# Kernel tuning notes

Hardware: AMD Instinct MI355X
Metric: run time of the kernel (lower is better)

The kernel has to match this reference:

```python
import jax, jax.numpy as jnp
import numpy as np

B, S, D_MODEL = 2, 2048, 2048
N_HEADS, N_KV_HEADS = 32, 8
HEAD_DIM = D_MODEL // N_HEADS  # 64


def setup_inputs() -> dict:
    key = jax.random.key(0)
    ks = jax.random.split(key, 7)
    # rope frequencies (as in standard RoPE; values just need to be the right shape)
    inv_freq = 1.0 / (10000.0 ** (jnp.arange(0, HEAD_DIM, 2, dtype=jnp.float32) / HEAD_DIM))
    t = jnp.arange(S, dtype=jnp.float32)
    freqs = t[:, None] * inv_freq[None, :]  # (S, head_dim//2)
    scale = 0.02
    return {
        "x": jax.random.normal(ks[0], (B, S, D_MODEL), jnp.float32),
        "cos": jnp.cos(freqs),
        "sin": jnp.sin(freqs),
        "Wq": jax.random.normal(ks[1], (N_HEADS * HEAD_DIM, D_MODEL), jnp.float32) * scale,
        "Wk": jax.random.normal(ks[2], (N_KV_HEADS * HEAD_DIM, D_MODEL), jnp.float32) * scale,
        "Wv": jax.random.normal(ks[3], (N_KV_HEADS * HEAD_DIM, D_MODEL), jnp.float32) * scale,
        "Wo": jax.random.normal(ks[4], (D_MODEL, D_MODEL), jnp.float32) * scale,
    }


def _apply_rope(x, cos, sin):
    # x: (B, H, S, D); cos/sin: (S, D//2)
    d = x.shape[-1]
    x1, x2 = x[..., : d // 2], x[..., d // 2:]
    c = cos[None, None]
    s = sin[None, None]
    return jnp.concatenate([x1 * c - x2 * s, x1 * s + x2 * c], axis=-1)


def reference(x, cos, sin, Wq, Wk, Wv, Wo):
    b, s, _ = x.shape
    hd = 2 * cos.shape[-1]
    h = Wq.shape[0] // hd
    kv = Wk.shape[0] // hd
    g = h // kv  # query heads per kv head

    q = (x @ Wq.T).reshape(b, s, h, hd).transpose(0, 2, 1, 3)    # (b,h,s,d)
    k = (x @ Wk.T).reshape(b, s, kv, hd).transpose(0, 2, 1, 3)   # (b,kv,s,d)
    v = (x @ Wv.T).reshape(b, s, kv, hd).transpose(0, 2, 1, 3)

    q = _apply_rope(q, cos, sin)
    k = _apply_rope(k, cos, sin)

    # GQA: group query heads instead of materializing repeated K/V
    qg = q.reshape(b, kv, g, s, hd)
    scale = 1.0 / jnp.sqrt(jnp.asarray(hd, x.dtype))
    scores = jnp.einsum('bkgsd,bktd->bkgst', qg, k) * scale      # (b,kv,g,s,s)
    causal = jnp.arange(s)[:, None] >= jnp.arange(s)[None, :]
    scores = jnp.where(causal[None, None, None], scores, jnp.asarray(-jnp.inf, scores.dtype))
    attn = jax.nn.softmax(scores, axis=-1)
    out = jnp.einsum('bkgst,bktd->bkgsd', attn, v)               # (b,kv,g,s,d)
    out = out.reshape(b, h, s, hd).transpose(0, 2, 1, 3).reshape(b, s, h * hd)
    return out @ Wo.T
```

## Files before the change

### kernel.cpp

```cpp
#include <hip/hip_runtime.h>
#include <hip/hip_bf16.h>

typedef __bf16 bf16;
typedef __attribute__((ext_vector_type(8))) __bf16 bf16x8;
typedef __attribute__((ext_vector_type(4))) __bf16 bf16x4;
typedef __attribute__((ext_vector_type(4))) float f32x4;

#define B_SZ 2
#define S_SZ 2048
#define D_SZ 2048
#define H_SZ 32
#define KV_SZ 8
#define HD_SZ 64
#define M_SZ (B_SZ * S_SZ)
#define NQKV 3072

#define GLDS(g, s) __builtin_amdgcn_global_load_lds( \
    (const __attribute__((address_space(1))) void*)(g), \
    (__attribute__((address_space(3))) void*)(s), 16, 0, 0)

__global__ void cvt_all(const float* __restrict__ x, const float* __restrict__ Wq,
                        const float* __restrict__ Wk, const float* __restrict__ Wv,
                        const float* __restrict__ Wo,
                        bf16* __restrict__ xb, bf16* __restrict__ Wf, bf16* __restrict__ wob,
                        int nx, int n1, int n2) {
    int i = blockIdx.x * blockDim.x + threadIdx.x;
    const float* src; bf16* dst; int off;
    if (i < nx)                 { src = x;  dst = xb; off = i; }
    else {
        int j = i - nx;
        if (j < n1)             { src = Wq; dst = Wf; off = j; }
        else if (j < n1 + n2)   { src = Wk; dst = Wf + (size_t)4 * n1; off = j - n1; }
        else if (j < n1 + 2*n2) { src = Wv; dst = Wf + (size_t)4 * (n1 + n2); off = j - n1 - n2; }
        else if (j < 2*n1+2*n2) { src = Wo; dst = wob; off = j - n1 - 2 * n2; }
        else return;
    }
    float4 v = ((const float4*)src)[off];
    bf16x4 o;
    o.x = (bf16)v.x; o.y = (bf16)v.y; o.z = (bf16)v.z; o.w = (bf16)v.w;
    ((bf16x4*)dst)[off] = o;
}

#define GEMM_CORE2(A_, B_, Kdim)                                                 \
    const int tid  = threadIdx.x;                                                \
    const int w    = tid >> 6;                                                   \
    const int lane = tid & 63;                                                   \
    const int c = lane & 15, quad = lane >> 4;                                   \
    const int g8 = lane >> 3;                                                    \
    const int chs = ((lane & 7) ^ g8) * 8;                                       \
    const int rowBase = blockIdx.y * 128;                                        \
    const int colBase = blockIdx.x * 128;                                        \
    const bf16* Ag = A_ + (size_t)(rowBase + w * 64 + g8) * Kdim + chs;          \
    const bf16* Bg = B_ + (size_t)(colBase + w * 64 + g8) * Kdim + chs;          \
    bf16* sAw = As + (w * 64) * 64;                                              \
    bf16* sBw = Bs + (w * 64) * 64;                                              \
    f32x4 acc[4][8] = {};                                                        \
    for (int k0 = 0; k0 < Kdim; k0 += 64) {                                      \
        _Pragma("unroll")                                                        \
        for (int j = 0; j < 8; j++) {                                            \
            GLDS(Ag + (size_t)(j * 8) * Kdim + k0, sAw + j * 512);               \
            GLDS(Bg + (size_t)(j * 8) * Kdim + k0, sBw + j * 512);               \
        }                                                                        \
        __syncthreads();                                                         \
        _Pragma("unroll")                                                        \
        for (int ks = 0; ks < 2; ks++) {                                         \
            bf16x8 af[4], bfr[8];                                                \
            _Pragma("unroll")                                                    \
            for (int mi = 0; mi < 4; mi++)                                       \
                af[mi] = *(const bf16x8*)(As + (w * 64 + mi * 16 + c) * 64       \
                                          + (((ks << 2) + quad) ^ (c & 7)) * 8); \
            _Pragma("unroll")                                                    \
            for (int ni = 0; ni < 8; ni++)                                       \
                bfr[ni] = *(const bf16x8*)(Bs + (ni * 16 + c) * 64               \
                                          + (((ks << 2) + quad) ^ (c & 7)) * 8); \
            _Pragma("unroll")                                                    \
            for (int mi = 0; mi < 4; mi++)                                       \
                _Pragma("unroll")                                                \
                for (int ni = 0; ni < 8; ni++)                                   \
                    acc[mi][ni] = __builtin_amdgcn_mfma_f32_16x16x32_bf16(       \
                        af[mi], bfr[ni], acc[mi][ni], 0, 0, 0);                  \
        }                                                                        \
        __syncthreads();                                                         \
    }                                                                            \
    const int mBase = rowBase + w * 64;

__global__ __launch_bounds__(128, 2)
void gemm_qkv(const bf16* __restrict__ A, const bf16* __restrict__ Bw,
              bf16* __restrict__ Qb, bf16* __restrict__ Kb, bf16* __restrict__ Vtb,
              const float* __restrict__ cosp, const float* __restrict__ sinp,
              float qscale)
{
    __shared__ __align__(16) bf16 As[128 * 64];
    __shared__ __align__(16) bf16 Bs[128 * 64];

    GEMM_CORE2(A, Bw, D_SZ)

#pragma unroll
    for (int half = 0; half < 2; half++) {
        const int hcol = colBase + half * 64;
        const int no   = half * 4;
        if (hcol < 2560) {
            bf16* dst; int hh, Hn; float sc;
            if (hcol < 2048) { dst = Qb; hh = hcol >> 6;        Hn = H_SZ;  sc = qscale; }
            else             { dst = Kb; hh = (hcol >> 6) - 32; Hn = KV_SZ; sc = 1.0f;  }
#pragma unroll
            for (int mi = 0; mi < 4; mi++) {
#pragma unroll
                for (int r = 0; r < 4; r++) {
                    int row = mBase + mi * 16 + quad * 4 + r;
                    int b = row >> 11;
                    int s = row & 2047;
                    const float* cr = cosp + (size_t)s * 32;
                    const float* sr = sinp + (size_t)s * 32;
                    size_t base = ((size_t)(b * Hn + hh) * S_SZ + s) * 64;
#pragma unroll
                    for (int nj = 0; nj < 2; nj++) {
                        int d = nj * 16 + c;
                        float x1 = acc[mi][no + nj][r];
                        float x2 = acc[mi][no + nj + 2][r];
                        float cv = cr[d], sv = sr[d];
                        dst[base + d]      = (bf16)((x1 * cv - x2 * sv) * sc);
                        dst[base + d + 32] = (bf16)((x1 * sv + x2 * cv) * sc);
                    }
                }
            }
        } else {
            const int kvh = (hcol >> 6) - 40;
            const int b   = mBase >> 11;
            const int s0  = mBase & 2047;
#pragma unroll
            for (int nj = 0; nj < 4; nj++) {
                int d = nj * 16 + c;
                size_t base = ((size_t)(b * KV_SZ + kvh) * 64 + d) * (size_t)S_SZ;
#pragma unroll
                for (int mi = 0; mi < 4; mi++) {
                    int s = s0 + mi * 16 + quad * 4;
#pragma unroll
                    for (int r = 0; r < 4; r++)
                        Vtb[base + s + r] = (bf16)acc[mi][no + nj][r];
                }
            }
        }
    }
}

__global__ __launch_bounds__(128, 2)
void gemm_out(const bf16* __restrict__ A, const bf16* __restrict__ Bw,
              float* __restrict__ Co, int N, int K)
{
    __shared__ __align__(16) bf16 As[128 * 64];
    __shared__ __align__(16) bf16 Bs[128 * 64];

    GEMM_CORE2(A, Bw, K)

#pragma unroll
    for (int mi = 0; mi < 4; mi++)
#pragma unroll
        for (int ni = 0; ni < 8; ni++) {
            int col = colBase + ni * 16 + c;
#pragma unroll
            for (int r = 0; r < 4; r++) {
                int row = mBase + mi * 16 + quad * 4 + r;
                Co[(size_t)row * N + col] = acc[mi][ni][r];
            }
        }
}

#define PST 72

__global__ __launch_bounds__(256, 3)
void flash_attn(const bf16* __restrict__ Q, const bf16* __restrict__ Kc,
                const bf16* __restrict__ Vt, bf16* __restrict__ Aout)
{
    __shared__ __align__(16) bf16 Ks[64 * 64];
    __shared__ __align__(16) bf16 Vs[64 * 64];
    __shared__ __align__(16) bf16 Ps[2 * 4 * 16 * PST];

    const int tid  = threadIdx.x;
    const int lane = tid & 63;
    const int wave = tid >> 6;
    const int c = lane & 15, quad = lane >> 4;
    const int qloc = wave * 16 + c;

    const int i  = blockIdx.x;
    const int tA = 31 - i, tB = i;
    const int q0A = tA << 6, q0B = tB << 6;

    const int bh = blockIdx.y;
    const int b  = bh >> 5;
    const int h  = bh & 31;
    const int kv = h >> 2;

    const bf16* Qp = Q  + (size_t)bh * (S_SZ * 64);
    const bf16* Kp = Kc + (size_t)(b * KV_SZ + kv) * (S_SZ * 64);
    const bf16* Vp = Vt + (size_t)(b * KV_SZ + kv) * (64 * S_SZ);

    bf16x8 aqA[2], aqB[2];
    {
        const bf16* qa = Qp + (size_t)(q0A + qloc) * 64 + quad * 8;
        aqA[0] = *(const bf16x8*)qa;  aqA[1] = *(const bf16x8*)(qa + 32);
        const bf16* qb = Qp + (size_t)(q0B + qloc) * 64 + quad * 8;
        aqB[0] = *(const bf16x8*)qb;  aqB[1] = *(const bf16x8*)(qb + 32);
    }

    f32x4 oA[4] = {}, oB[4] = {};
    f32x4 lA = {}, lB = {};

    bf16x8 ones;
#pragma unroll
    for (int j = 0; j < 8; j++) ones[j] = (bf16)1.0f;

    const int srow = tid >> 3;
    const int ch   = tid & 7;
    const int sws  = (ch ^ (srow & 7)) * 8;
    const bf16* Kg0 = Kp + (size_t)srow * 64 + ch * 8;
    const bf16* Kg1 = Kp + (size_t)(srow + 32) * 64 + ch * 8;
    const bf16* Vg0 = Vp + (size_t)srow * S_SZ + ch * 8;
    const bf16* Vg1 = Vp + (size_t)(srow + 32) * S_SZ + ch * 8;

    uint4 pk0 = *(const uint4*)Kg0, pk1 = *(const uint4*)Kg1;
    uint4 pv0 = *(const uint4*)Vg0, pv1 = *(const uint4*)Vg1;

    bf16* PwA = Ps + wave * 16 * PST;
    bf16* PwB = Ps + (4 + wave) * 16 * PST;

    for (int kt = 0; kt <= tA; kt++) {
        *(uint4*)(Ks + srow * 64 + sws)        = pk0;
        *(uint4*)(Ks + (srow + 32) * 64 + sws) = pk1;
        *(uint4*)(Vs + srow * 64 + sws)        = pv0;
        *(uint4*)(Vs + (srow + 32) * 64 + sws) = pv1;
        __syncthreads();
        if (kt < tA) {
            pk0 = *(const uint4*)(Kg0 + (size_t)(kt + 1) * 4096);
            pk1 = *(const uint4*)(Kg1 + (size_t)(kt + 1) * 4096);
            pv0 = *(const uint4*)(Vg0 + (kt + 1) * 64);
            pv1 = *(const uint4*)(Vg1 + (kt + 1) * 64);
        }

        bf16x8 ak[2][4], av[2][4];
#pragma unroll
        for (int ks = 0; ks < 2; ks++)
#pragma unroll
            for (int ni = 0; ni < 4; ni++) {
                const int co = (((ks << 2) + quad) ^ (c & 7)) * 8;
                ak[ks][ni] = *(const bf16x8*)(Ks + (ni * 16 + c) * 64 + co);
                av[ks][ni] = *(const bf16x8*)(Vs + (ni * 16 + c) * 64 + co);
            }

        const bool diagA = (kt == tA);
        const bool doB   = (kt <= tB);
        const bool diagB = (kt == tB);

        {
            f32x4 sc[4] = {};
#pragma unroll
            for (int ks = 0; ks < 2; ks++)
#pragma unroll
                for (int ni = 0; ni < 4; ni++)
                    sc[ni] = __builtin_amdgcn_mfma_f32_16x16x32_bf16(ak[ks][ni], aqA[ks], sc[ni], 0, 0, 0);
#pragma unroll
            for (int ni = 0; ni < 4; ni++) {
                bf16x4 pk;
#pragma unroll
                for (int r = 0; r < 4; r++) {
                    float p = exp2f(sc[ni][r]);
                    if (diagA && (ni * 16 + quad * 4 + r) > qloc) p = 0.f;
                    pk[r] = (bf16)p;
                }
                *(bf16x4*)(PwA + c * PST + ni * 16 + quad * 4) = pk;
            }
#pragma unroll
            for (int ks = 0; ks < 2; ks++) {
                bf16x8 bp = *(const bf16x8*)(PwA + c * PST + ks * 32 + quad * 8);
                lA = __builtin_amdgcn_mfma_f32_16x16x32_bf16(ones, bp, lA, 0, 0, 0);
#pragma unroll
                for (int ni = 0; ni < 4; ni++)
                    oA[ni] = __builtin_amdgcn_mfma_f32_16x16x32_bf16(av[ks][ni], bp, oA[ni], 0, 0, 0);
            }
        }
        if (doB) {
            f32x4 sc[4] = {};
#pragma unroll
            for (int ks = 0; ks < 2; ks++)
#pragma unroll
                for (int ni = 0; ni < 4; ni++)
                    sc[ni] = __builtin_amdgcn_mfma_f32_16x16x32_bf16(ak[ks][ni], aqB[ks], sc[ni], 0, 0, 0);
#pragma unroll
            for (int ni = 0; ni < 4; ni++) {
                bf16x4 pk;
#pragma unroll
                for (int r = 0; r < 4; r++) {
                    float p = exp2f(sc[ni][r]);
                    if (diagB && (ni * 16 + quad * 4 + r) > qloc) p = 0.f;
                    pk[r] = (bf16)p;
                }
                *(bf16x4*)(PwB + c * PST + ni * 16 + quad * 4) = pk;
            }
#pragma unroll
            for (int ks = 0; ks < 2; ks++) {
                bf16x8 bp = *(const bf16x8*)(PwB + c * PST + ks * 32 + quad * 8);
                lB = __builtin_amdgcn_mfma_f32_16x16x32_bf16(ones, bp, lB, 0, 0, 0);
#pragma unroll
                for (int ni = 0; ni < 4; ni++)
                    oB[ni] = __builtin_amdgcn_mfma_f32_16x16x32_bf16(av[ks][ni], bp, oB[ni], 0, 0, 0);
            }
        }
        __syncthreads();
    }

    {
        float ila = 1.f / lA[0];
        float ilb = 1.f / lB[0];
        bf16* pa = Aout + ((size_t)(b * S_SZ + q0A + qloc)) * D_SZ + h * 64;
        bf16* pb = Aout + ((size_t)(b * S_SZ + q0B + qloc)) * D_SZ + h * 64;
#pragma unroll
        for (int ni = 0; ni < 4; ni++) {
            bf16x4 wa, wb;
#pragma unroll
            for (int r = 0; r < 4; r++) {
                wa[r] = (bf16)(oA[ni][r] * ila);
                wb[r] = (bf16)(oB[ni][r] * ilb);
            }
            *(bf16x4*)(pa + ni * 16 + quad * 4) = wa;
            *(bf16x4*)(pb + ni * 16 + quad * 4) = wb;
        }
    }
}

extern "C" void kernel_launch(void* const* d_in, const int* in_sizes, int n_in,
                              void* d_out, int out_size, void* d_ws, size_t ws_size,
                              hipStream_t stream) {
    const float* x    = (const float*)d_in[0];
    const float* cosp = (const float*)d_in[1];
    const float* sinp = (const float*)d_in[2];
    const float* Wq   = (const float*)d_in[3];
    const float* Wk   = (const float*)d_in[4];
    const float* Wv   = (const float*)d_in[5];
    const float* Wo   = (const float*)d_in[6];
    float* out = (float*)d_out;

    const int M = M_SZ;
    const int D = D_SZ;
    const int NKV = KV_SZ * HD_SZ;

    bf16* xb   = (bf16*)d_ws;
    bf16* Wf   = xb  + (size_t)M * D;
    bf16* Qb   = Wf  + (size_t)NQKV * D;
    bf16* Kb   = Qb  + (size_t)M * D;
    bf16* Vtb  = Kb  + (size_t)B_SZ * KV_SZ * S_SZ * 64;
    bf16* wob  = Vtb + (size_t)B_SZ * KV_SZ * 64 * S_SZ;
    bf16* attn = xb;

    const int nx = M * D / 4, n1 = D * D / 4, n2 = NKV * D / 4;

    cvt_all<<<(nx + 2 * n1 + 2 * n2 + 255) / 256, 256, 0, stream>>>(
        x, Wq, Wk, Wv, Wo, xb, Wf, wob, nx, n1, n2);

    const float qscale = 0.125f * 1.44269504089f;

    gemm_qkv<<<dim3(NQKV / 128, M / 128), 128, 0, stream>>>(xb, Wf, Qb, Kb, Vtb, cosp, sinp, qscale);

    flash_attn<<<dim3(16, B_SZ * H_SZ), 256, 0, stream>>>(Qb, Kb, Vtb, attn);

    gemm_out<<<dim3(D / 128, M / 128), 128, 0, stream>>>(attn, wob, out, D, D);
}
```

Before: 294.1 us.

## Widen flash-attention query tiles to 128 rows per tile pair for K/V reuse

Each workgroup now processes two 128-row query tiles (paired causally as 15-i and i), with each wave handling 32 query rows. Each K/V tile loaded into LDS is therefore reused across twice as many queries, halving K/V traffic and sync overhead per query. The grid drops to 8 x 64 workgroups and launch bounds fall to 2 per SIMD. The change also adds MFMA s_setprio hints and moves V fragment loads after the QK/softmax step. The risks are higher register pressure, lower occupancy, and fewer workgroups to fill the device.

```diff
diff --git a/kernel.cpp b/kernel.cpp
--- a/kernel.cpp
+++ b/kernel.cpp
@@ -168,23 +168,26 @@
 
 #define PST 72
 
-__global__ __launch_bounds__(256, 3)
+__global__ __launch_bounds__(256, 2)
 void flash_attn(const bf16* __restrict__ Q, const bf16* __restrict__ Kc,
                 const bf16* __restrict__ Vt, bf16* __restrict__ Aout)
 {
     __shared__ __align__(16) bf16 Ks[64 * 64];
     __shared__ __align__(16) bf16 Vs[64 * 64];
-    __shared__ __align__(16) bf16 Ps[2 * 4 * 16 * PST];
+    __shared__ __align__(16) bf16 Ps[256 * PST];
 
     const int tid  = threadIdx.x;
     const int lane = tid & 63;
     const int wave = tid >> 6;
     const int c = lane & 15, quad = lane >> 4;
-    const int qloc = wave * 16 + c;
-
-    const int i  = blockIdx.x;
-    const int tA = 31 - i, tB = i;
-    const int q0A = tA << 6, q0B = tB << 6;
+
+    const int i   = blockIdx.x;
+    const int tA  = 15 - i, tB = i;
+    const int qA0 = tA << 7, qB0 = tB << 7;
+    const int ktEnd = 2 * tA + 1;
+    const int ktB   = 2 * tB + 1;
+    const int mA0   = 2 * tA;
+    const int mB0   = 2 * tB;
 
     const int bh = blockIdx.y;
     const int b  = bh >> 5;
@@ -195,16 +198,21 @@
     const bf16* Kp = Kc + (size_t)(b * KV_SZ + kv) * (S_SZ * 64);
     const bf16* Vp = Vt + (size_t)(b * KV_SZ + kv) * (64 * S_SZ);
 
-    bf16x8 aqA[2], aqB[2];
-    {
-        const bf16* qa = Qp + (size_t)(q0A + qloc) * 64 + quad * 8;
-        aqA[0] = *(const bf16x8*)qa;  aqA[1] = *(const bf16x8*)(qa + 32);
-        const bf16* qb = Qp + (size_t)(q0B + qloc) * 64 + quad * 8;
-        aqB[0] = *(const bf16x8*)qb;  aqB[1] = *(const bf16x8*)(qb + 32);
-    }
-
-    f32x4 oA[4] = {}, oB[4] = {};
-    f32x4 lA = {}, lB = {};
+    const int wq = wave * 32;
+
+    bf16x8 aqA[2][2], aqB[2][2];
+#pragma unroll
+    for (int qb = 0; qb < 2; qb++) {
+        const bf16* qa = Qp + (size_t)(qA0 + wq + qb * 16 + c) * 64 + quad * 8;
+        aqA[qb][0] = *(const bf16x8*)qa;
+        aqA[qb][1] = *(const bf16x8*)(qa + 32);
+        const bf16* qbp = Qp + (size_t)(qB0 + wq + qb * 16 + c) * 64 + quad * 8;
+        aqB[qb][0] = *(const bf16x8*)qbp;
+        aqB[qb][1] = *(const bf16x8*)(qbp + 32);
+    }
+
+    f32x4 oA[2][4] = {}, oB[2][4] = {};
+    f32x4 lA[2] = {}, lB[2] = {};
 
     bf16x8 ones;
 #pragma unroll
@@ -221,105 +229,105 @@
     uint4 pk0 = *(const uint4*)Kg0, pk1 = *(const uint4*)Kg1;
     uint4 pv0 = *(const uint4*)Vg0, pv1 = *(const uint4*)Vg1;
 
-    bf16* PwA = Ps + wave * 16 * PST;
-    bf16* PwB = Ps + (4 + wave) * 16 * PST;
-
-    for (int kt = 0; kt <= tA; kt++) {
+    bf16* Pw = Ps + ((size_t)wave * 64 + c) * PST;
+
+#define QK_SM(AQ, TQ, QG0, MFROM)                                              \
+    _Pragma("unroll")                                                          \
+    for (int qb = 0; qb < 2; qb++) {                                           \
+        f32x4 sc[4] = {};                                                      \
+        __builtin_amdgcn_s_setprio(1);                                         \
+        _Pragma("unroll")                                                      \
+        for (int ks = 0; ks < 2; ks++)                                         \
+            _Pragma("unroll")                                                  \
+            for (int ni = 0; ni < 4; ni++)                                     \
+                sc[ni] = __builtin_amdgcn_mfma_f32_16x16x32_bf16(              \
+                    ak[ks][ni], AQ[qb][ks], sc[ni], 0, 0, 0);                  \
+        __builtin_amdgcn_s_setprio(0);                                         \
+        const int qg = (QG0) + wq + qb * 16 + c;                               \
+        bf16* pdst = Pw + ((TQ) * 2 + qb) * (16 * PST);                        \
+        const bool msk = (kt >= (MFROM));                                      \
+        _Pragma("unroll")                                                      \
+        for (int ni = 0; ni < 4; ni++) {                                       \
+            bf16x4 pk;                                                         \
+            _Pragma("unroll")                                                  \
+            for (int r = 0; r < 4; r++) {                                      \
+                float p = exp2f(sc[ni][r]);                                    \
+                if (msk && (kt * 64 + ni * 16 + quad * 4 + r) > qg) p = 0.f;   \
+                pk[r] = (bf16)p;                                               \
+            }                                                                  \
+            *(bf16x4*)(pdst + ni * 16 + quad * 4) = pk;                        \
+        }                                                                      \
+    }
+
+#define PV_ACC(TQ, OACC, LACC)                                                 \
+    _Pragma("unroll")                                                          \
+    for (int qb = 0; qb < 2; qb++) {                                           \
+        const bf16* psrc = Pw + ((TQ) * 2 + qb) * (16 * PST);                  \
+        _Pragma("unroll")                                                      \
+        for (int ks = 0; ks < 2; ks++) {                                       \
+            bf16x8 bp = *(const bf16x8*)(psrc + ks * 32 + quad * 8);           \
+            __builtin_amdgcn_s_setprio(1);                                     \
+            LACC[qb] = __builtin_amdgcn_mfma_f32_16x16x32_bf16(                \
+                ones, bp, LACC[qb], 0, 0, 0);                                  \
+            _Pragma("unroll")                                                  \
+            for (int ni = 0; ni < 4; ni++)                                     \
+                OACC[qb][ni] = __builtin_amdgcn_mfma_f32_16x16x32_bf16(        \
+                    av[ks][ni], bp, OACC[qb][ni], 0, 0, 0);                    \
+            __builtin_amdgcn_s_setprio(0);                                     \
+        }                                                                      \
+    }
+
+    for (int kt = 0; kt <= ktEnd; kt++) {
         *(uint4*)(Ks + srow * 64 + sws)        = pk0;
         *(uint4*)(Ks + (srow + 32) * 64 + sws) = pk1;
         *(uint4*)(Vs + srow * 64 + sws)        = pv0;
         *(uint4*)(Vs + (srow + 32) * 64 + sws) = pv1;
         __syncthreads();
-        if (kt < tA) {
+        if (kt < ktEnd) {
             pk0 = *(const uint4*)(Kg0 + (size_t)(kt + 1) * 4096);
             pk1 = *(const uint4*)(Kg1 + (size_t)(kt + 1) * 4096);
             pv0 = *(const uint4*)(Vg0 + (kt + 1) * 64);
             pv1 = *(const uint4*)(Vg1 + (kt + 1) * 64);
         }
-
-        bf16x8 ak[2][4], av[2][4];
+        const bool doB = (kt <= ktB);
+
+        bf16x8 ak[2][4];
 #pragma unroll
         for (int ks = 0; ks < 2; ks++)
 #pragma unroll
-            for (int ni = 0; ni < 4; ni++) {
-                const int co = (((ks << 2) + quad) ^ (c & 7)) * 8;
-                ak[ks][ni] = *(const bf16x8*)(Ks + (ni * 16 + c) * 64 + co);
-                av[ks][ni] = *(const bf16x8*)(Vs + (ni * 16 + c) * 64 + co);
-            }
-
-        const bool diagA = (kt == tA);
-        const bool doB   = (kt <= tB);
-        const bool diagB = (kt == tB);
-
-        {
-            f32x4 sc[4] = {};
-#pragma unroll
-            for (int ks = 0; ks < 2; ks++)
-#pragma unroll
-                for (int ni = 0; ni < 4; ni++)
-                    sc[ni] = __builtin_amdgcn_mfma_f32_16x16x32_bf16(ak[ks][ni], aqA[ks], sc[ni], 0, 0, 0);
-#pragma unroll
-            for (int ni = 0; ni < 4; ni++) {
-                bf16x4 pk;
-#pragma unroll
-                for (int r = 0; r < 4; r++) {
-                    float p = exp2f(sc[ni][r]);
-                    if (diagA && (ni * 16 + quad * 4 + r) > qloc) p = 0.f;
-                    pk[r] = (bf16)p;
-                }
-                *(bf16x4*)(PwA + c * PST + ni * 16 + quad * 4) = pk;
-            }
-#pragma unroll
-            for (int ks = 0; ks < 2; ks++) {
-                bf16x8 bp = *(const bf16x8*)(PwA + c * PST + ks * 32 + quad * 8);
-                lA = __builtin_amdgcn_mfma_f32_16x16x32_bf16(ones, bp, lA, 0, 0, 0);
-#pragma unroll
-                for (int ni = 0; ni < 4; ni++)
-                    oA[ni] = __builtin_amdgcn_mfma_f32_16x16x32_bf16(av[ks][ni], bp, oA[ni], 0, 0, 0);
-            }
-        }
-        if (doB) {
-            f32x4 sc[4] = {};
-#pragma unroll
-            for (int ks = 0; ks < 2; ks++)
-#pragma unroll
-                for (int ni = 0; ni < 4; ni++)
-                    sc[ni] = __builtin_amdgcn_mfma_f32_16x16x32_bf16(ak[ks][ni], aqB[ks], sc[ni], 0, 0, 0);
-#pragma unroll
-            for (int ni = 0; ni < 4; ni++) {
-                bf16x4 pk;
-#pragma unroll
-                for (int r = 0; r < 4; r++) {
-                    float p = exp2f(sc[ni][r]);
-                    if (diagB && (ni * 16 + quad * 4 + r) > qloc) p = 0.f;
-                    pk[r] = (bf16)p;
-                }
-                *(bf16x4*)(PwB + c * PST + ni * 16 + quad * 4) = pk;
-            }
-#pragma unroll
-            for (int ks = 0; ks < 2; ks++) {
-                bf16x8 bp = *(const bf16x8*)(PwB + c * PST + ks * 32 + quad * 8);
-                lB = __builtin_amdgcn_mfma_f32_16x16x32_bf16(ones, bp, lB, 0, 0, 0);
-#pragma unroll
-                for (int ni = 0; ni < 4; ni++)
-                    oB[ni] = __builtin_amdgcn_mfma_f32_16x16x32_bf16(av[ks][ni], bp, oB[ni], 0, 0, 0);
-            }
-        }
+            for (int ni = 0; ni < 4; ni++)
+                ak[ks][ni] = *(const bf16x8*)(Ks + (ni * 16 + c) * 64
+                                              + (((ks << 2) + quad) ^ (c & 7)) * 8);
+
+        QK_SM(aqA, 0, qA0, mA0)
+        if (doB) { QK_SM(aqB, 1, qB0, mB0) }
+
+        bf16x8 av[2][4];
+#pragma unroll
+        for (int ks = 0; ks < 2; ks++)
+#pragma unroll
+            for (int ni = 0; ni < 4; ni++)
+                av[ks][ni] = *(const bf16x8*)(Vs + (ni * 16 + c) * 64
+                                              + (((ks << 2) + quad) ^ (c & 7)) * 8);
+
+        PV_ACC(0, oA, lA)
+        if (doB) { PV_ACC(1, oB, lB) }
         __syncthreads();
     }
 
-    {
-        float ila = 1.f / lA[0];
-        float ilb = 1.f / lB[0];
-        bf16* pa = Aout + ((size_t)(b * S_SZ + q0A + qloc)) * D_SZ + h * 64;
-        bf16* pb = Aout + ((size_t)(b * S_SZ + q0B + qloc)) * D_SZ + h * 64;
+#pragma unroll
+    for (int qb = 0; qb < 2; qb++) {
+        float ila = 1.f / lA[qb][0];
+        float ilb = 1.f / lB[qb][0];
+        bf16* pa = Aout + ((size_t)(b * S_SZ + qA0 + wq + qb * 16 + c)) * D_SZ + h * 64;
+        bf16* pb = Aout + ((size_t)(b * S_SZ + qB0 + wq + qb * 16 + c)) * D_SZ + h * 64;
 #pragma unroll
         for (int ni = 0; ni < 4; ni++) {
             bf16x4 wa, wb;
 #pragma unroll
             for (int r = 0; r < 4; r++) {
-                wa[r] = (bf16)(oA[ni][r] * ila);
-                wb[r] = (bf16)(oB[ni][r] * ilb);
+                wa[r] = (bf16)(oA[qb][ni][r] * ila);
+                wb[r] = (bf16)(oB[qb][ni][r] * ilb);
             }
             *(bf16x4*)(pa + ni * 16 + quad * 4) = wa;
             *(bf16x4*)(pb + ni * 16 + quad * 4) = wb;
@@ -360,7 +368,7 @@
 
     gemm_qkv<<<dim3(NQKV / 128, M / 128), 128, 0, stream>>>(xb, Wf, Qb, Kb, Vtb, cosp, sinp, qscale);
 
-    flash_attn<<<dim3(16, B_SZ * H_SZ), 256, 0, stream>>>(Qb, Kb, Vtb, attn);
+    flash_attn<<<dim3(8, B_SZ * H_SZ), 256, 0, stream>>>(Qb, Kb, Vtb, attn);
 
     gemm_out<<<dim3(D / 128, M / 128), 128, 0, stream>>>(attn, wob, out, D, D);
 }
```

Result: no change. 296.5 us (+0.8%).

## Restructure flash attention loop to cut register pressure and raise occupancy

Applied to the files above, without the earlier changes.

Instead of preloading all K and V fragments at once, the attention inner loop loads K fragments per k-step and V fragments later, just before the PV MFMAs. This lowers register use so launch bounds can go from 3 to 4 blocks per SM. The QK MFMAs for both query tiles are interleaved, the diagonal masking branch is hoisted out of the exp loop, and s_setprio is raised around MFMA bursts. Barriers become an inline lgkmcnt wait plus s_barrier issued after the next-tile global prefetch. The risk is that the custom barrier skips waiting on vmcnt, and forcing 4 blocks per SM may cause spills.

```diff
diff --git a/kernel.cpp b/kernel.cpp
--- a/kernel.cpp
+++ b/kernel.cpp
@@ -18,6 +18,10 @@
 #define GLDS(g, s) __builtin_amdgcn_global_load_lds( \
     (const __attribute__((address_space(1))) void*)(g), \
     (__attribute__((address_space(3))) void*)(s), 16, 0, 0)
+
+__device__ __forceinline__ void bar_lgkm() {
+    asm volatile("s_waitcnt lgkmcnt(0)\n\ts_barrier" ::: "memory");
+}
 
 __global__ void cvt_all(const float* __restrict__ x, const float* __restrict__ Wq,
                         const float* __restrict__ Wk, const float* __restrict__ Wv,
@@ -168,7 +172,7 @@
 
 #define PST 72
 
-__global__ __launch_bounds__(256, 3)
+__global__ __launch_bounds__(256, 4)
 void flash_attn(const bf16* __restrict__ Q, const bf16* __restrict__ Kc,
                 const bf16* __restrict__ Vt, bf16* __restrict__ Aout)
 {
@@ -229,83 +233,108 @@
         *(uint4*)(Ks + (srow + 32) * 64 + sws) = pk1;
         *(uint4*)(Vs + srow * 64 + sws)        = pv0;
         *(uint4*)(Vs + (srow + 32) * 64 + sws) = pv1;
-        __syncthreads();
         if (kt < tA) {
             pk0 = *(const uint4*)(Kg0 + (size_t)(kt + 1) * 4096);
             pk1 = *(const uint4*)(Kg1 + (size_t)(kt + 1) * 4096);
             pv0 = *(const uint4*)(Vg0 + (kt + 1) * 64);
             pv1 = *(const uint4*)(Vg1 + (kt + 1) * 64);
         }
-
-        bf16x8 ak[2][4], av[2][4];
-#pragma unroll
-        for (int ks = 0; ks < 2; ks++)
-#pragma unroll
-            for (int ni = 0; ni < 4; ni++) {
-                const int co = (((ks << 2) + quad) ^ (c & 7)) * 8;
-                ak[ks][ni] = *(const bf16x8*)(Ks + (ni * 16 + c) * 64 + co);
-                av[ks][ni] = *(const bf16x8*)(Vs + (ni * 16 + c) * 64 + co);
-            }
-
+        bar_lgkm();
+
+        const bool doB   = (kt <= tB);
         const bool diagA = (kt == tA);
-        const bool doB   = (kt <= tB);
         const bool diagB = (kt == tB);
 
-        {
-            f32x4 sc[4] = {};
-#pragma unroll
-            for (int ks = 0; ks < 2; ks++)
+        f32x4 scA[4] = {}, scB[4] = {};
+#pragma unroll
+        for (int ks = 0; ks < 2; ks++) {
+            bf16x8 ak4[4];
+#pragma unroll
+            for (int ni = 0; ni < 4; ni++)
+                ak4[ni] = *(const bf16x8*)(Ks + (ni * 16 + c) * 64
+                                           + (((ks << 2) + quad) ^ (c & 7)) * 8);
+            __builtin_amdgcn_s_setprio(1);
+#pragma unroll
+            for (int ni = 0; ni < 4; ni++)
+                scA[ni] = __builtin_amdgcn_mfma_f32_16x16x32_bf16(ak4[ni], aqA[ks], scA[ni], 0, 0, 0);
+            if (doB) {
 #pragma unroll
                 for (int ni = 0; ni < 4; ni++)
-                    sc[ni] = __builtin_amdgcn_mfma_f32_16x16x32_bf16(ak[ks][ni], aqA[ks], sc[ni], 0, 0, 0);
+                    scB[ni] = __builtin_amdgcn_mfma_f32_16x16x32_bf16(ak4[ni], aqB[ks], scB[ni], 0, 0, 0);
+            }
+            __builtin_amdgcn_s_setprio(0);
+        }
+
+        if (diagA) {
 #pragma unroll
             for (int ni = 0; ni < 4; ni++) {
                 bf16x4 pk;
 #pragma unroll
                 for (int r = 0; r < 4; r++) {
-                    float p = exp2f(sc[ni][r]);
-                    if (diagA && (ni * 16 + quad * 4 + r) > qloc) p = 0.f;
+                    float p = exp2f(scA[ni][r]);
+                    if ((ni * 16 + quad * 4 + r) > qloc) p = 0.f;
                     pk[r] = (bf16)p;
                 }
                 *(bf16x4*)(PwA + c * PST + ni * 16 + quad * 4) = pk;
             }
-#pragma unroll
-            for (int ks = 0; ks < 2; ks++) {
-                bf16x8 bp = *(const bf16x8*)(PwA + c * PST + ks * 32 + quad * 8);
-                lA = __builtin_amdgcn_mfma_f32_16x16x32_bf16(ones, bp, lA, 0, 0, 0);
-#pragma unroll
-                for (int ni = 0; ni < 4; ni++)
-                    oA[ni] = __builtin_amdgcn_mfma_f32_16x16x32_bf16(av[ks][ni], bp, oA[ni], 0, 0, 0);
-            }
-        }
-        if (doB) {
-            f32x4 sc[4] = {};
-#pragma unroll
-            for (int ks = 0; ks < 2; ks++)
-#pragma unroll
-                for (int ni = 0; ni < 4; ni++)
-                    sc[ni] = __builtin_amdgcn_mfma_f32_16x16x32_bf16(ak[ks][ni], aqB[ks], sc[ni], 0, 0, 0);
+        } else {
 #pragma unroll
             for (int ni = 0; ni < 4; ni++) {
                 bf16x4 pk;
 #pragma unroll
-                for (int r = 0; r < 4; r++) {
-                    float p = exp2f(sc[ni][r]);
-                    if (diagB && (ni * 16 + quad * 4 + r) > qloc) p = 0.f;
-                    pk[r] = (bf16)p;
-                }
-                *(bf16x4*)(PwB + c * PST + ni * 16 + quad * 4) = pk;
-            }
-#pragma unroll
-            for (int ks = 0; ks < 2; ks++) {
-                bf16x8 bp = *(const bf16x8*)(PwB + c * PST + ks * 32 + quad * 8);
-                lB = __builtin_amdgcn_mfma_f32_16x16x32_bf16(ones, bp, lB, 0, 0, 0);
+                for (int r = 0; r < 4; r++) pk[r] = (bf16)exp2f(scA[ni][r]);
+                *(bf16x4*)(PwA + c * PST + ni * 16 + quad * 4) = pk;
+            }
+        }
+        if (doB) {
+            if (diagB) {
+#pragma unroll
+                for (int ni = 0; ni < 4; ni++) {
+                    bf16x4 pk;
+#pragma unroll
+                    for (int r = 0; r < 4; r++) {
+                        float p = exp2f(scB[ni][r]);
+                        if ((ni * 16 + quad * 4 + r) > qloc) p = 0.f;
+                        pk[r] = (bf16)p;
+                    }
+                    *(bf16x4*)(PwB + c * PST + ni * 16 + quad * 4) = pk;
+                }
+            } else {
+#pragma unroll
+                for (int ni = 0; ni < 4; ni++) {
+                    bf16x4 pk;
+#pragma unroll
+                    for (int r = 0; r < 4; r++) pk[r] = (bf16)exp2f(scB[ni][r]);
+                    *(bf16x4*)(PwB + c * PST + ni * 16 + quad * 4) = pk;
+                }
+            }
+        }
+
+#pragma unroll
+        for (int ks = 0; ks < 2; ks++) {
+            bf16x8 av4[4];
+#pragma unroll
+            for (int ni = 0; ni < 4; ni++)
+                av4[ni] = *(const bf16x8*)(Vs + (ni * 16 + c) * 64
+                                           + (((ks << 2) + quad) ^ (c & 7)) * 8);
+            bf16x8 bpA = *(const bf16x8*)(PwA + c * PST + ks * 32 + quad * 8);
+            __builtin_amdgcn_s_setprio(1);
+            lA = __builtin_amdgcn_mfma_f32_16x16x32_bf16(ones, bpA, lA, 0, 0, 0);
+#pragma unroll
+            for (int ni = 0; ni < 4; ni++)
+                oA[ni] = __builtin_amdgcn_mfma_f32_16x16x32_bf16(av4[ni], bpA, oA[ni], 0, 0, 0);
+            __builtin_amdgcn_s_setprio(0);
+            if (doB) {
+                bf16x8 bpB = *(const bf16x8*)(PwB + c * PST + ks * 32 + quad * 8);
+                __builtin_amdgcn_s_setprio(1);
+                lB = __builtin_amdgcn_mfma_f32_16x16x32_bf16(ones, bpB, lB, 0, 0, 0);
 #pragma unroll
                 for (int ni = 0; ni < 4; ni++)
-                    oB[ni] = __builtin_amdgcn_mfma_f32_16x16x32_bf16(av[ks][ni], bp, oB[ni], 0, 0, 0);
-            }
-        }
-        __syncthreads();
+                    oB[ni] = __builtin_amdgcn_mfma_f32_16x16x32_bf16(av4[ni], bpB, oB[ni], 0, 0, 0);
+                __builtin_amdgcn_s_setprio(0);
+            }
+        }
+        bar_lgkm();
     }
 
     {
```

New measurement: 405.9 us. +38.0%, slower.
